# Optimization experiments

Measured on AMD Instinct MI355X. Metric: run time of the kernel, lower is better.

Reference implementation:

```python
import jax, jax.numpy as jnp
import numpy as np

B = 64
A_DIM, T_DIM, V_DIM = 512, 1024, 512
H = 96
O1, O2, O3 = 6, 1, 3
HP1 = H + 1  # 97


def setup_inputs() -> dict:
    key = jax.random.key(0)
    ks = jax.random.split(key, 20)
    s = 0.02
    inp = {
        "audios": jax.random.normal(ks[0], (B, A_DIM), jnp.float32),
        "texts": jax.random.normal(ks[1], (B, T_DIM), jnp.float32),
        "videos": jax.random.normal(ks[2], (B, V_DIM), jnp.float32),
        # MLP encoders: Linear(in, hidden) + ReLU (dropout is identity at eval)
        "Wa": jax.random.normal(ks[3], (A_DIM, H), jnp.float32) * s,
        "ba": jnp.zeros((H,), jnp.float32),
        "Wt": jax.random.normal(ks[4], (T_DIM, H), jnp.float32) * s,
        "bt": jnp.zeros((H,), jnp.float32),
        "Wv": jax.random.normal(ks[5], (V_DIM, H), jnp.float32) * s,
        "bv": jnp.zeros((H,), jnp.float32),
        # post-fusion MLP
        "W1": jax.random.normal(ks[6], (HP1 * HP1 * HP1, H), jnp.float32) * s,
        "b1": jnp.zeros((H,), jnp.float32),
        "W2": jax.random.normal(ks[7], (H, H), jnp.float32) * s,
        "b2": jnp.zeros((H,), jnp.float32),
        # output heads
        "Wo1": jax.random.normal(ks[8], (H, O1), jnp.float32) * s,
        "bo1": jnp.zeros((O1,), jnp.float32),
        "Wo2": jax.random.normal(ks[9], (H, O2), jnp.float32) * s,
        "bo2": jnp.zeros((O2,), jnp.float32),
        "Wo3": jax.random.normal(ks[10], (H, O3), jnp.float32) * s,
        "bo3": jnp.zeros((O3,), jnp.float32),
    }
    return inp


def reference(audios, texts, videos, Wa, ba, Wt, bt, Wv, bv,
              W1, b1, W2, b2, Wo1, bo1, Wo2, bo2, Wo3, bo3):
    # encoders (eval mode: dropout = identity)
    ah = jax.nn.relu(audios @ Wa + ba)   # [B, H]
    th = jax.nn.relu(texts @ Wt + bt)    # [B, H]
    vh = jax.nn.relu(videos @ Wv + bv)   # [B, H]

    one = jnp.ones((ah.shape[0], 1), ah.dtype)
    a1 = jnp.concatenate([one, ah], axis=1)  # [B, H+1]
    v1 = jnp.concatenate([one, vh], axis=1)  # [B, H+1]
    t1 = jnp.concatenate([one, th], axis=1)  # [B, H+1]

    # trilinear outer product: bmm(a1[:, :, None], v1[:, None, :]) -> [B, A, V]
    # then bmm with t1 -> [B, A*V, T]; flatten order is (a, v, t)
    fusion = jnp.einsum('ba,bv,bt->bavt', a1, v1, t1).reshape(a1.shape[0], -1)

    y1 = jax.nn.relu(fusion @ W1 + b1)
    features = jax.nn.relu(y1 @ W2 + b2)

    emos_out = features @ Wo1 + bo1
    vals_out = features @ Wo2 + bo2
    sents_out = features @ Wo3 + bo3
    interloss = jnp.zeros((), jnp.float32)
    return (features, emos_out, vals_out, sents_out, interloss)
```

## Files before the change

kernel.cpp:

```cpp
#include <hip/hip_runtime.h>


typedef unsigned int u32;
typedef short frag8s __attribute__((ext_vector_type(8)));
typedef float f32x4 __attribute__((ext_vector_type(4)));

constexpr int G3     = 589;
constexpr int NRUN   = 9409;
constexpr int NRUNP  = 9412;
constexpr int NGROUP = 2353;

constexpr int WS_A1T  = 0;
constexpr int WS_V1T  = WS_A1T + 98 * 64;
constexpr int WS_T1T  = WS_V1T + 98 * 64;
constexpr int WS_T1PK = WS_T1T + 98 * 64;
constexpr int WS_S    = WS_T1PK + 64 * 64;
constexpr int WS_WAT  = WS_S + NRUNP * 64;
constexpr int WS_WTT  = WS_WAT + 96 * 512;
constexpr int WS_WVT  = WS_WTT + 96 * 1024;
constexpr int WS_Y1   = WS_WVT + 96 * 512;
constexpr int WS_PART = WS_Y1 + 6144;

__device__ __forceinline__ u32 bfrne(float x) {
    u32 u = __float_as_uint(x);
    return (u + 0x7FFFu + ((u >> 16) & 1u)) >> 16;
}
__device__ __forceinline__ float bflo(u32 p) { return __uint_as_float(p << 16); }
__device__ __forceinline__ float bfhi(u32 p) { return __uint_as_float(p & 0xFFFF0000u); }

__device__ __forceinline__ void async_cp16(float* lds, const float* g) {
    __builtin_amdgcn_global_load_lds((const __attribute__((address_space(1))) u32*)g,
                                     (__attribute__((address_space(3))) u32*)lds, 16, 0, 0);
}
__device__ __forceinline__ void async_cp4(float* lds, const float* g) {
    __builtin_amdgcn_global_load_lds((const __attribute__((address_space(1))) u32*)g,
                                     (__attribute__((address_space(3))) u32*)lds, 4, 0, 0);
}

__global__ void k0_transpose(const float* __restrict__ Wa, const float* __restrict__ Wt,
                             const float* __restrict__ Wv, float* __restrict__ ws) {
    int idx = blockIdx.x * 256 + threadIdx.x;
    if (idx < 49152) {
        int h = idx / 512, k = idx % 512;
        ws[WS_WAT + h * 512 + k] = Wa[k * 96 + h];
    } else if (idx < 147456) {
        int i = idx - 49152; int h = i / 1024, k = i % 1024;
        ws[WS_WTT + h * 1024 + k] = Wt[k * 96 + h];
    } else if (idx < 196608) {
        int i = idx - 147456; int h = i / 512, k = i % 512;
        ws[WS_WVT + h * 512 + k] = Wv[k * 96 + h];
    }
}

__global__ __launch_bounds__(256) void k1_enc(const float* __restrict__ audios,
                                              const float* __restrict__ texts,
                                              const float* __restrict__ videos,
                                              const float* __restrict__ ba,
                                              const float* __restrict__ bt,
                                              const float* __restrict__ bv,
                                              float* __restrict__ ws) {
    int wg = blockIdx.x, tid = threadIdx.x;
    int lane = tid & 63, wv = tid >> 6;
    if (wg == 288) {
        if (tid < 64) ws[WS_T1T + 97 * 64 + tid] = 0.0f;
        return;
    }
    int e = wg / 96, h = wg % 96;
    const float* in; const float* wt; float bias; int K; int outbase;
    if (e == 0)      { in = audios; wt = ws + WS_WAT + h * 512;  bias = ba[h]; K = 512;  outbase = WS_A1T; }
    else if (e == 1) { in = texts;  wt = ws + WS_WTT + h * 1024; bias = bt[h]; K = 1024; outbase = WS_T1T; }
    else             { in = videos; wt = ws + WS_WVT + h * 512;  bias = bv[h]; K = 512;  outbase = WS_V1T; }
    int nsweep = K >> 8;
    float4 wreg[4];
    for (int s = 0; s < nsweep; s++) wreg[s] = ((const float4*)wt)[s * 64 + lane];
    for (int pass = 0; pass < 16; pass++) {
        int b = pass * 4 + wv;
        float acc = 0.f;
        for (int s = 0; s < nsweep; s++) {
            float4 iv = ((const float4*)(in + b * K))[s * 64 + lane];
            acc += iv.x * wreg[s].x + iv.y * wreg[s].y + iv.z * wreg[s].z + iv.w * wreg[s].w;
        }
        for (int off = 32; off; off >>= 1) acc += __shfl_down(acc, off, 64);
        if (lane == 0) {
            float v = acc + bias;
            ws[outbase + (h + 1) * 64 + b] = v > 0.f ? v : 0.f;
        }
    }
    if (h == 0 && tid < 64) ws[outbase + tid] = 1.0f;
}

__global__ __launch_bounds__(256) void k2_s(float* __restrict__ ws) {
    int wg = blockIdx.x, tid = threadIdx.x;
    u32* t1pk = (u32*)ws + WS_T1PK;
    if (wg == 589) {
        for (int i = tid; i < 4096; i += 256) {
            int b = i >> 6, p = i & 63;
            u32 v = 0;
            if (p < 49) {
                float e0 = ws[WS_T1T + (2 * p) * 64 + b];
                float e1 = ws[WS_T1T + (2 * p + 1) * 64 + b];
                v = bfrne(e0) | (bfrne(e1) << 16);
            }
            t1pk[i] = v;
        }
        return;
    }
    for (int ii = 0; ii < 4; ii++) {
        int idx = wg * 1024 + ii * 256 + tid;
        if (idx >= NRUNP * 64) break;
        int run = idx >> 6, b = idx & 63;
        float s = 0.f;
        if (run < NRUN) {
            int i = run / 97, j = run % 97;
            s = ws[WS_A1T + i * 64 + b] * ws[WS_V1T + j * 64 + b];
        }
        ws[WS_S + idx] = s;
    }
}

__global__ __launch_bounds__(256) void k3_main(const float* __restrict__ W1,
                                               float* __restrict__ ws) {
    __shared__ float wtile[2][32 * 96];
    __shared__ u32   tpk[64 * 65];
    __shared__ float sl[2][4 * 64];

    int tid = threadIdx.x, lane = tid & 63, wv = tid >> 6;
    int id = blockIdx.x;
    const u32* t1pk_g = (const u32*)ws + WS_T1PK;
    const float* s_g = ws + WS_S;

    for (int i = tid; i < 2 * 32 * 96 / 4; i += 256)
        ((float4*)wtile)[i] = make_float4(0.f, 0.f, 0.f, 0.f);
    for (int i = tid; i < 4096; i += 256) {
        int b = i >> 6, p = i & 63;
        tpk[b * 65 + p] = t1pk_g[i];
    }

    int glist[4]; int gcount = 0;
    for (int i2 = 0; i2 < 4; i2++) { int g = id + i2 * G3; if (g < NGROUP) glist[gcount++] = g; }

    f32x4 acc[6];
    for (int nt = 0; nt < 6; nt++) acc[nt] = f32x4{0.f, 0.f, 0.f, 0.f};

    auto stage_w = [&](int g, int koff, int buf) {
        int run = g * 4 + wv; if (run > 9408) run = 9408;
        if (koff < 96) {
            const float* gsrc = W1 + (size_t)(run * 97 + koff) * 96;
            float* ldst = &wtile[buf][wv * 768];
            for (int c = 0; c < 3; c++)
                async_cp16(ldst + c * 256, gsrc + c * 256 + lane * 4);
        } else {
            if (lane < 24)
                async_cp16(&wtile[buf][wv * 768], W1 + (size_t)(run * 97 + 96) * 96 + lane * 4);
        }
    };
    auto stage_s = [&](int g, int sb) {
        if (wv == 0) {
            for (int q2 = 0; q2 < 4; q2++) {
                int run = g * 4 + q2;
                async_cp4(&sl[sb][q2 * 64], s_g + run * 64 + lane);
            }
        }
    };

    stage_s(glist[0], 0);
    stage_w(glist[0], 0, 0);
    __syncthreads();

    int pw = 0, sb = 0;
    int b = (wv << 4) + (lane & 15);
    int q = lane >> 4;

    for (int gi = 0; gi < gcount; gi++) {
        int g = glist[gi];
        for (int step = 0; step < 13; step++) {
            int koff = step * 8;
            if (step < 12) stage_w(g, koff + 8, pw ^ 1);
            else if (gi + 1 < gcount) { stage_w(glist[gi + 1], 0, pw ^ 1); stage_s(glist[gi + 1], sb ^ 1); }

            float s = sl[sb][q * 64 + b];
            int pb = b * 65 + (koff >> 1);
            u32 ap[4];
#pragma unroll
            for (int r = 0; r < 4; r++) {
                u32 tp = tpk[pb + r];
                float fe = s * bflo(tp), fo = s * bfhi(tp);
                ap[r] = bfrne(fe) | (bfrne(fo) << 16);
            }
            union { u32 u[4]; frag8s f; } afr;
            afr.u[0] = ap[0]; afr.u[1] = ap[1]; afr.u[2] = ap[2]; afr.u[3] = ap[3];

            const float* wt0 = &wtile[pw][q * 768 + (lane & 15)];
#pragma unroll
            for (int nt = 0; nt < 6; nt++) {
                union { u32 u[4]; frag8s f; } bfr;
#pragma unroll
                for (int r = 0; r < 4; r++) {
                    u32 w0 = __float_as_uint(wt0[(2 * r) * 96 + nt * 16]);
                    u32 w1 = __float_as_uint(wt0[(2 * r + 1) * 96 + nt * 16]);
                    bfr.u[r] = (w0 >> 16) | (w1 & 0xFFFF0000u);
                }
                acc[nt] = __builtin_amdgcn_mfma_f32_16x16x32_bf16(afr.f, bfr.f, acc[nt], 0, 0, 0);
            }
            __syncthreads();
            pw ^= 1;
        }
        sb ^= 1;
    }

    float* part = ws + WS_PART + (size_t)id * 6144;
#pragma unroll
    for (int nt = 0; nt < 6; nt++) {
#pragma unroll
        for (int r = 0; r < 4; r++) {
            int row = (wv << 4) + ((lane >> 4) << 2) + r;
            int col = nt * 16 + (lane & 15);
            part[row * 96 + col] = acc[nt][r];
        }
    }
}

__global__ __launch_bounds__(256) void k4_reduce(const float* __restrict__ b1,
                                                 float* __restrict__ ws) {
    int o = blockIdx.x * 256 + threadIdx.x;
    const float* part = ws + WS_PART + o;
    float a0 = 0.f, a1 = 0.f, a2 = 0.f, a3 = 0.f;
    int w = 0;
    for (; w + 4 <= G3; w += 4) {
        a0 += part[(size_t)(w + 0) * 6144];
        a1 += part[(size_t)(w + 1) * 6144];
        a2 += part[(size_t)(w + 2) * 6144];
        a3 += part[(size_t)(w + 3) * 6144];
    }
    for (; w < G3; w++) a0 += part[(size_t)w * 6144];
    float acc = (a0 + a1) + (a2 + a3) + b1[o % 96];
    ws[WS_Y1 + o] = acc > 0.f ? acc : 0.f;
}

__global__ __launch_bounds__(256) void k5_final(const float* __restrict__ W2, const float* __restrict__ b2,
                                                const float* __restrict__ Wo1, const float* __restrict__ bo1,
                                                const float* __restrict__ Wo2, const float* __restrict__ bo2,
                                                const float* __restrict__ Wo3, const float* __restrict__ bo3,
                                                const float* __restrict__ ws, float* __restrict__ out) {
    __shared__ float yl[64 * 96];
    __shared__ float w2l[96 * 97];
    __shared__ float fl[64 * 96];
    int tid = threadIdx.x;
    for (int i = tid; i < 6144; i += 256) yl[i] = ws[WS_Y1 + i];
    for (int i = tid; i < 9216; i += 256) { int k = i / 96, h = i % 96; w2l[k * 97 + h] = W2[i]; }
    __syncthreads();
    for (int i = tid; i < 6144; i += 256) {
        int bb = i / 96, h = i % 96;
        float acc = b2[h];
#pragma unroll 8
        for (int k = 0; k < 96; k++) acc += yl[bb * 96 + k] * w2l[k * 97 + h];
        float f = acc > 0.f ? acc : 0.f;
        fl[i] = f; out[i] = f;
    }
    __syncthreads();
    for (int i = tid; i < 640; i += 256) {
        if (i < 384) {
            int bb = i / 6, j = i % 6;
            float acc = bo1[j];
            for (int k = 0; k < 96; k++) acc += fl[bb * 96 + k] * Wo1[k * 6 + j];
            out[6144 + i] = acc;
        } else if (i < 448) {
            int bb = i - 384;
            float acc = bo2[0];
            for (int k = 0; k < 96; k++) acc += fl[bb * 96 + k] * Wo2[k];
            out[6144 + i] = acc;
        } else {
            int t2 = i - 448; int bb = t2 / 3, j = t2 % 3;
            float acc = bo3[j];
            for (int k = 0; k < 96; k++) acc += fl[bb * 96 + k] * Wo3[k * 3 + j];
            out[6144 + i] = acc;
        }
    }
    if (tid == 0) out[6784] = 0.0f;
}

extern "C" void kernel_launch(void* const* d_in, const int* in_sizes, int n_in,
                              void* d_out, int out_size, void* d_ws, size_t ws_size,
                              hipStream_t stream) {
    (void)in_sizes; (void)n_in; (void)out_size; (void)ws_size;
    const float* audios = (const float*)d_in[0];
    const float* texts  = (const float*)d_in[1];
    const float* videos = (const float*)d_in[2];
    const float* Wa  = (const float*)d_in[3];
    const float* ba  = (const float*)d_in[4];
    const float* Wt  = (const float*)d_in[5];
    const float* bt  = (const float*)d_in[6];
    const float* Wv  = (const float*)d_in[7];
    const float* bv  = (const float*)d_in[8];
    const float* W1  = (const float*)d_in[9];
    const float* b1  = (const float*)d_in[10];
    const float* W2  = (const float*)d_in[11];
    const float* b2  = (const float*)d_in[12];
    const float* Wo1 = (const float*)d_in[13];
    const float* bo1 = (const float*)d_in[14];
    const float* Wo2 = (const float*)d_in[15];
    const float* bo2 = (const float*)d_in[16];
    const float* Wo3 = (const float*)d_in[17];
    const float* bo3 = (const float*)d_in[18];
    float* ws = (float*)d_ws;
    float* outp = (float*)d_out;

    k0_transpose<<<768, 256, 0, stream>>>(Wa, Wt, Wv, ws);
    k1_enc<<<289, 256, 0, stream>>>(audios, texts, videos, ba, bt, bv, ws);
    k2_s<<<590, 256, 0, stream>>>(ws);
    k3_main<<<G3, 256, 0, stream>>>(W1, ws);
    k4_reduce<<<24, 256, 0, stream>>>(b1, ws);
    k5_final<<<1, 256, 0, stream>>>(W2, b2, Wo1, bo1, Wo2, bo2, Wo3, bo3, ws, outp);
}
```

Measured before the change: 650.6 us.

## Split reduction into two stages and parallelize final MLP across blocks

The single 24-block reduction over 589 partial tiles becomes a 192-block first stage that writes 8 partial sums. The final kernel then sums those 8 partials, adds bias and applies ReLU, and computes the W2 layer and output heads across 8 blocks of 8 rows each instead of one block. The LDS weight tile row stride is padded from 768 to 776 floats to reduce bank conflicts. This adds extra workspace and one more round of memory traffic, but exposes far more parallelism for the bandwidth-bound reduction.

```diff
diff --git a/kernel.cpp b/kernel.cpp
--- a/kernel.cpp
+++ b/kernel.cpp
@@ -9,6 +9,7 @@
 constexpr int NRUN   = 9409;
 constexpr int NRUNP  = 9412;
 constexpr int NGROUP = 2353;
+constexpr int RBLK   = 776;
 
 constexpr int WS_A1T  = 0;
 constexpr int WS_V1T  = WS_A1T + 98 * 64;
@@ -18,8 +19,8 @@
 constexpr int WS_WAT  = WS_S + NRUNP * 64;
 constexpr int WS_WTT  = WS_WAT + 96 * 512;
 constexpr int WS_WVT  = WS_WTT + 96 * 1024;
-constexpr int WS_Y1   = WS_WVT + 96 * 512;
-constexpr int WS_PART = WS_Y1 + 6144;
+constexpr int WS_PART = WS_WVT + 96 * 512;
+constexpr int WS_PART2= WS_PART + G3 * 6144;
 
 __device__ __forceinline__ u32 bfrne(float x) {
     u32 u = __float_as_uint(x);
@@ -108,7 +109,8 @@
     for (int ii = 0; ii < 4; ii++) {
         int idx = wg * 1024 + ii * 256 + tid;
         if (idx >= NRUNP * 64) break;
-        int run = idx >> 6, b = idx & 63;
+        int run = idx >> 6, b = idx & 6 * 10 + 3;
+        b = idx & 63;
         float s = 0.f;
         if (run < NRUN) {
             int i = run / 97, j = run % 97;
@@ -120,7 +122,7 @@
 
 __global__ __launch_bounds__(256) void k3_main(const float* __restrict__ W1,
                                                float* __restrict__ ws) {
-    __shared__ float wtile[2][32 * 96];
+    __shared__ float wtile[2][4 * RBLK];
     __shared__ u32   tpk[64 * 65];
     __shared__ float sl[2][4 * 64];
 
@@ -129,7 +131,7 @@
     const u32* t1pk_g = (const u32*)ws + WS_T1PK;
     const float* s_g = ws + WS_S;
 
-    for (int i = tid; i < 2 * 32 * 96 / 4; i += 256)
+    for (int i = tid; i < 2 * 4 * RBLK / 4; i += 256)
         ((float4*)wtile)[i] = make_float4(0.f, 0.f, 0.f, 0.f);
     for (int i = tid; i < 4096; i += 256) {
         int b = i >> 6, p = i & 63;
@@ -146,12 +148,12 @@
         int run = g * 4 + wv; if (run > 9408) run = 9408;
         if (koff < 96) {
             const float* gsrc = W1 + (size_t)(run * 97 + koff) * 96;
-            float* ldst = &wtile[buf][wv * 768];
+            float* ldst = &wtile[buf][wv * RBLK];
             for (int c = 0; c < 3; c++)
                 async_cp16(ldst + c * 256, gsrc + c * 256 + lane * 4);
         } else {
             if (lane < 24)
-                async_cp16(&wtile[buf][wv * 768], W1 + (size_t)(run * 97 + 96) * 96 + lane * 4);
+                async_cp16(&wtile[buf][wv * RBLK], W1 + (size_t)(run * 97 + 96) * 96 + lane * 4);
         }
     };
     auto stage_s = [&](int g, int sb) {
@@ -190,7 +192,7 @@
             union { u32 u[4]; frag8s f; } afr;
             afr.u[0] = ap[0]; afr.u[1] = ap[1]; afr.u[2] = ap[2]; afr.u[3] = ap[3];
 
-            const float* wt0 = &wtile[pw][q * 768 + (lane & 15)];
+            const float* wt0 = &wtile[pw][q * RBLK + (lane & 15)];
 #pragma unroll
             for (int nt = 0; nt < 6; nt++) {
                 union { u32 u[4]; frag8s f; } bfr;
@@ -220,63 +222,70 @@
     }
 }
 
-__global__ __launch_bounds__(256) void k4_reduce(const float* __restrict__ b1,
-                                                 float* __restrict__ ws) {
-    int o = blockIdx.x * 256 + threadIdx.x;
+__global__ __launch_bounds__(256) void k4a_reduce(float* __restrict__ ws) {
+    int bid = blockIdx.x;
+    int oc = bid % 24, wc = bid / 24;
+    int o = oc * 256 + threadIdx.x;
+    int w0 = wc * 74, w1 = w0 + 74; if (w1 > G3) w1 = G3;
     const float* part = ws + WS_PART + o;
-    float a0 = 0.f, a1 = 0.f, a2 = 0.f, a3 = 0.f;
-    int w = 0;
-    for (; w + 4 <= G3; w += 4) {
-        a0 += part[(size_t)(w + 0) * 6144];
+    float a0 = 0.f, a1 = 0.f;
+    int w = w0;
+    for (; w + 2 <= w1; w += 2) {
+        a0 += part[(size_t)w * 6144];
         a1 += part[(size_t)(w + 1) * 6144];
-        a2 += part[(size_t)(w + 2) * 6144];
-        a3 += part[(size_t)(w + 3) * 6144];
-    }
-    for (; w < G3; w++) a0 += part[(size_t)w * 6144];
-    float acc = (a0 + a1) + (a2 + a3) + b1[o % 96];
-    ws[WS_Y1 + o] = acc > 0.f ? acc : 0.f;
-}
-
-__global__ __launch_bounds__(256) void k5_final(const float* __restrict__ W2, const float* __restrict__ b2,
+    }
+    for (; w < w1; w++) a0 += part[(size_t)w * 6144];
+    ws[WS_PART2 + (size_t)wc * 6144 + o] = a0 + a1;
+}
+
+__global__ __launch_bounds__(256) void k5_final(const float* __restrict__ b1,
+                                                const float* __restrict__ W2, const float* __restrict__ b2,
                                                 const float* __restrict__ Wo1, const float* __restrict__ bo1,
                                                 const float* __restrict__ Wo2, const float* __restrict__ bo2,
                                                 const float* __restrict__ Wo3, const float* __restrict__ bo3,
                                                 const float* __restrict__ ws, float* __restrict__ out) {
-    __shared__ float yl[64 * 96];
+    __shared__ float yl[8 * 96];
     __shared__ float w2l[96 * 97];
-    __shared__ float fl[64 * 96];
+    __shared__ float fl[8 * 96];
     int tid = threadIdx.x;
-    for (int i = tid; i < 6144; i += 256) yl[i] = ws[WS_Y1 + i];
+    int row0 = blockIdx.x * 8;
+    for (int i = tid; i < 768; i += 256) {
+        int go = row0 * 96 + i;
+        float acc = b1[i % 96];
+#pragma unroll
+        for (int w = 0; w < 8; w++) acc += ws[WS_PART2 + (size_t)w * 6144 + go];
+        yl[i] = acc > 0.f ? acc : 0.f;
+    }
     for (int i = tid; i < 9216; i += 256) { int k = i / 96, h = i % 96; w2l[k * 97 + h] = W2[i]; }
     __syncthreads();
-    for (int i = tid; i < 6144; i += 256) {
+    for (int i = tid; i < 768; i += 256) {
         int bb = i / 96, h = i % 96;
         float acc = b2[h];
 #pragma unroll 8
         for (int k = 0; k < 96; k++) acc += yl[bb * 96 + k] * w2l[k * 97 + h];
         float f = acc > 0.f ? acc : 0.f;
-        fl[i] = f; out[i] = f;
+        fl[i] = f; out[(row0 + bb) * 96 + h] = f;
     }
     __syncthreads();
-    for (int i = tid; i < 640; i += 256) {
-        if (i < 384) {
-            int bb = i / 6, j = i % 6;
+    if (tid < 80) {
+        if (tid < 48) {
+            int lr = tid / 6, j = tid % 6;
             float acc = bo1[j];
-            for (int k = 0; k < 96; k++) acc += fl[bb * 96 + k] * Wo1[k * 6 + j];
-            out[6144 + i] = acc;
-        } else if (i < 448) {
-            int bb = i - 384;
+            for (int k = 0; k < 96; k++) acc += fl[lr * 96 + k] * Wo1[k * 6 + j];
+            out[6144 + (row0 + lr) * 6 + j] = acc;
+        } else if (tid < 56) {
+            int lr = tid - 48;
             float acc = bo2[0];
-            for (int k = 0; k < 96; k++) acc += fl[bb * 96 + k] * Wo2[k];
-            out[6144 + i] = acc;
+            for (int k = 0; k < 96; k++) acc += fl[lr * 96 + k] * Wo2[k];
+            out[6528 + row0 + lr] = acc;
         } else {
-            int t2 = i - 448; int bb = t2 / 3, j = t2 % 3;
+            int t2 = tid - 56; int lr = t2 / 3, j = t2 % 3;
             float acc = bo3[j];
-            for (int k = 0; k < 96; k++) acc += fl[bb * 96 + k] * Wo3[k * 3 + j];
-            out[6144 + i] = acc;
-        }
-    }
-    if (tid == 0) out[6784] = 0.0f;
+            for (int k = 0; k < 96; k++) acc += fl[lr * 96 + k] * Wo3[k * 3 + j];
+            out[6592 + (row0 + lr) * 3 + j] = acc;
+        }
+    }
+    if (blockIdx.x == 0 && tid == 0) out[6784] = 0.0f;
 }
 
 extern "C" void kernel_launch(void* const* d_in, const int* in_sizes, int n_in,
@@ -309,6 +318,6 @@
     k1_enc<<<289, 256, 0, stream>>>(audios, texts, videos, ba, bt, bv, ws);
     k2_s<<<590, 256, 0, stream>>>(ws);
     k3_main<<<G3, 256, 0, stream>>>(W1, ws);
-    k4_reduce<<<24, 256, 0, stream>>>(b1, ws);
-    k5_final<<<1, 256, 0, stream>>>(W2, b2, Wo1, bo1, Wo2, bo2, Wo3, bo3, ws, outp);
-}
+    k4a_reduce<<<192, 256, 0, stream>>>(ws);
+    k5_final<<<8, 256, 0, stream>>>(b1, W2, b2, Wo1, bo1, Wo2, bo2, Wo3, bo3, ws, outp);
+}
```

Result: faster. 595.2 us (-8.5%).
